# Performance work log

Measured on AMD Instinct MI355X. Metric: run time of the kernel, lower is better.

Reference implementation:

```python
import jax, jax.numpy as jnp
import numpy as np

N_NODES = 50000
N_EDGES = 800000
D = 128
HEADS = 1
N_LAYERS = 3
NEG_SLOPE = 0.2


def setup_inputs() -> dict:
    key = jax.random.key(0)
    ks = jax.random.split(key, 8)
    x = jax.random.normal(ks[0], (N_NODES, D), dtype=jnp.float32)
    edge_index = jax.random.randint(ks[1], (2, N_EDGES), 0, N_NODES, dtype=jnp.int64)
    # Per-layer GATConv params (heads=1): lin [D, H*D], att_src/att_dst [H, D], bias [H*D]
    s = 1.0 / np.sqrt(D)
    W = jax.random.normal(ks[2], (N_LAYERS, D, HEADS * D), dtype=jnp.float32) * s
    att_src = jax.random.normal(ks[3], (N_LAYERS, HEADS, D), dtype=jnp.float32) * s
    att_dst = jax.random.normal(ks[4], (N_LAYERS, HEADS, D), dtype=jnp.float32) * s
    bias = jnp.zeros((N_LAYERS, HEADS * D), dtype=jnp.float32)
    return {"x": x, "edge_index": edge_index, "W": W, "att_src": att_src,
            "att_dst": att_dst, "bias": bias}


def _gat_conv(x, src, dst, W, a_src, a_dst, b):
    # x: [N, D] -> xp: [N, H, C]
    N = x.shape[0]
    xp = (x @ W).reshape(N, HEADS, D)
    alpha_s = jnp.sum(xp * a_src, axis=-1)  # [N, H]
    alpha_d = jnp.sum(xp * a_dst, axis=-1)  # [N, H]
    # per-edge attention logits (message j=src -> i=dst)
    e = alpha_s[src] + alpha_d[dst]                       # [E, H]
    e = jnp.where(e > 0, e, NEG_SLOPE * e)                # leaky_relu(0.2)
    # segment softmax over destination node
    m = jax.ops.segment_max(e, dst, num_segments=N)       # [N, H]
    ex = jnp.exp(e - m[dst])
    denom = jax.ops.segment_sum(ex, dst, num_segments=N)  # [N, H]
    coef = ex / (denom[dst] + 1e-16)                      # [E, H]
    # scatter-aggregate messages
    out = jax.ops.segment_sum(xp[src] * coef[:, :, None], dst, num_segments=N)  # [N, H, C]
    return out.reshape(N, HEADS * D) + b


def reference(x, edge_index, W, att_src, att_dst, bias):
    N = x.shape[0]
    # GATConv default add_self_loops=True: append (i, i) for every node
    loops = jnp.arange(N, dtype=edge_index.dtype)
    src = jnp.concatenate([edge_index[0], loops])
    dst = jnp.concatenate([edge_index[1], loops])
    h = x
    for l in range(N_LAYERS):
        # dropout omitted for deterministic reference (eval-mode semantics)
        h = _gat_conv(h, src, dst, W[l], att_src[l], att_dst[l], bias[l])
        if l < N_LAYERS - 1:
            h = jax.nn.gelu(h)
    return h
```

## Files before the change

### kernel.cpp

```cpp
#include <hip/hip_runtime.h>
#include <hip/hip_bf16.h>
#include <hip/hip_fp16.h>

#define NN    50000
#define NE    800000
#define ETOT  (NE + NN)
#define D     128
#define NB    ((NN + 255) / 256)
#define EB    ((ETOT + 255) / 256)

typedef _Float16 f16x8 __attribute__((ext_vector_type(8)));
typedef float    f32x4 __attribute__((ext_vector_type(4)));

__device__ __forceinline__ float gelu_fast(float x) {
    float x2 = x * x;
    float z2 = x * fmaf(x2, 0.07135483f, 1.5957691f);
    float e  = __expf(z2);
    return x - __fdividef(x, e + 1.0f);
}


__global__ __launch_bounds__(256) void init_k(
        int* __restrict__ counts, const float* __restrict__ W,
        const float* __restrict__ asrc, const float* __restrict__ adst,
        float* __restrict__ wasd, __half* __restrict__ WT) {
    int b = blockIdx.x, t = threadIdx.x;
    if (b < NB) {
        int i = b * 256 + t;
        if (i < NN) counts[i] = 0;
    } else if (b < NB + 3) {
        int l = b - NB;
        int k = t & 127, which = t >> 7;
        const float* wr = W + (size_t)l * 16384 + (size_t)k * 128;
        const float* av = (which ? adst : asrc) + (size_t)l * 128;
        float s = 0.f;
        #pragma unroll 4
        for (int c = 0; c < 128; ++c) s += wr[c] * av[c];
        wasd[l * 256 + which * 128 + k] = s;
    } else {
        int i = (b - NB - 3) * 256 + t;
        int l = i >> 14, r = i & 16383;
        int k = r >> 7, c = r & 127;
        WT[(size_t)l * 16384 + (size_t)c * 128 + k] =
            __float2half_rn(W[(size_t)l * 16384 + (size_t)k * 128 + c]);
    }
}


template <int AIN32>
__device__ __forceinline__ void gemm_body(
        int b2, int t, const void* __restrict__ A, const __half* __restrict__ WT,
        const float* __restrict__ wasd, __half* __restrict__ XP,
        float* __restrict__ alpha_s, float* __restrict__ alpha_d, __half* Bs) {
    #pragma unroll
    for (int it = 0; it < 8; ++it) {
        int bb = it * 4096 + t * 16;
        int c = bb >> 8;
        int swz = bb ^ ((c & 7) << 4);
        *(uint4*)((char*)Bs + swz) = *(const uint4*)((const char*)WT + bb);
    }
    __syncthreads();

    int w = t >> 6, lane = t & 63;
    int r0 = (b2 >> 1) * 256 + w * 64;
    int c0 = (b2 & 1) * 64;
    int lr = lane & 15, lg = lane >> 4;
    bool doalpha = (b2 & 1) == 0;

    f32x4 acc[4][4];
    #pragma unroll
    for (int i = 0; i < 4; ++i)
        #pragma unroll
        for (int j = 0; j < 4; ++j)
            acc[i][j] = (f32x4){0.f, 0.f, 0.f, 0.f};

    float ps[4] = {0, 0, 0, 0}, pd[4] = {0, 0, 0, 0};

    #pragma unroll
    for (int ks = 0; ks < 4; ++ks) {
        f16x8 bf[4];
        #pragma unroll
        for (int ct = 0; ct < 4; ++ct) {
            int c  = c0 + ct * 16 + lr;
            int kb = ks * 64 + lg * 16;
            int addr = c * 256 + (kb ^ ((c & 7) << 4));
            bf[ct] = *(const f16x8*)((const char*)Bs + addr);
        }
        float4 s0, s1, d0, d1;
        if (doalpha) {
            const float* wsp = wasd + ks * 32 + lg * 8;
            s0 = *(const float4*)(wsp);       s1 = *(const float4*)(wsp + 4);
            d0 = *(const float4*)(wsp + 128); d1 = *(const float4*)(wsp + 132);
        }
        #pragma unroll
        for (int rt = 0; rt < 4; ++rt) {
            int row = r0 + rt * 16 + lr;
            int rc  = row < NN ? row : NN - 1;
            f16x8 af;
            float4 f0, f1;
            if (AIN32) {
                const float* ap = (const float*)A + (size_t)rc * D + ks * 32 + lg * 8;
                f0 = *(const float4*)ap;
                f1 = *(const float4*)(ap + 4);
                af[0] = (_Float16)f0.x; af[1] = (_Float16)f0.y;
                af[2] = (_Float16)f0.z; af[3] = (_Float16)f0.w;
                af[4] = (_Float16)f1.x; af[5] = (_Float16)f1.y;
                af[6] = (_Float16)f1.z; af[7] = (_Float16)f1.w;
            } else {
                af = *(const f16x8*)((const char*)A + (size_t)rc * 256 + ks * 64 + lg * 16);
                if (doalpha) {
                    f0 = make_float4((float)af[0], (float)af[1], (float)af[2], (float)af[3]);
                    f1 = make_float4((float)af[4], (float)af[5], (float)af[6], (float)af[7]);
                }
            }
            if (doalpha) {
                ps[rt] += f0.x*s0.x + f0.y*s0.y + f0.z*s0.z + f0.w*s0.w
                        + f1.x*s1.x + f1.y*s1.y + f1.z*s1.z + f1.w*s1.w;
                pd[rt] += f0.x*d0.x + f0.y*d0.y + f0.z*d0.z + f0.w*d0.w
                        + f1.x*d1.x + f1.y*d1.y + f1.z*d1.z + f1.w*d1.w;
            }
            #pragma unroll
            for (int ct = 0; ct < 4; ++ct)
                acc[rt][ct] = __builtin_amdgcn_mfma_f32_16x16x32_f16(
                                  af, bf[ct], acc[rt][ct], 0, 0, 0);
        }
    }

    #pragma unroll
    for (int rt = 0; rt < 4; ++rt) {
        #pragma unroll
        for (int q = 0; q < 4; ++q) {
            int row = r0 + rt * 16 + lg * 4 + q;
            if (row < NN) {
                #pragma unroll
                for (int ct = 0; ct < 4; ++ct)
                    XP[(size_t)row * D + c0 + ct * 16 + lr] = __float2half_rn(acc[rt][ct][q]);
            }
        }
    }

    if (doalpha) {
        #pragma unroll
        for (int rt = 0; rt < 4; ++rt) {
            float p = ps[rt], dq = pd[rt];
            p  += __shfl_xor(p, 16);  p  += __shfl_xor(p, 32);
            dq += __shfl_xor(dq, 16); dq += __shfl_xor(dq, 32);
            int row = r0 + rt * 16 + lr;
            if (lane < 16 && row < NN) { alpha_s[row] = p; alpha_d[row] = dq; }
        }
    }
}


__global__ __launch_bounds__(256) void prep2_k(
        const int* __restrict__ dst_arr, int* __restrict__ counts, int* __restrict__ rank,
        const float* __restrict__ x, const __half* __restrict__ WT,
        const float* __restrict__ wasd, __half* __restrict__ XPH,
        float* __restrict__ alpha_s, float* __restrict__ alpha_d) {
    __shared__ __half Bs[D * D];
    int b = blockIdx.x, t = threadIdx.x;
    if (b < EB) {
        int e = b * 256 + t;
        if (e < ETOT) {
            int d = (e < NE) ? dst_arr[e] : (e - NE);
            rank[e] = atomicAdd(&counts[d], 1);
        }
    } else {
        gemm_body<1>(b - EB, t, x, WT, wasd, XPH, alpha_s, alpha_d, Bs);
    }
}


__global__ __launch_bounds__(256) void gemm_k(
        const __half* __restrict__ TH, const __half* __restrict__ WT,
        const float* __restrict__ wasd, __half* __restrict__ XPH,
        float* __restrict__ alpha_s, float* __restrict__ alpha_d) {
    __shared__ __half Bs[D * D];
    gemm_body<0>(blockIdx.x, threadIdx.x, TH, WT, wasd, XPH, alpha_s, alpha_d, Bs);
}


__global__ void scan1_k(const int* __restrict__ counts, int* __restrict__ blk_sums) {
    __shared__ int sm[4];
    int i = blockIdx.x * 256 + threadIdx.x;
    int v = (i < NN) ? counts[i] : 0;
    #pragma unroll
    for (int o = 32; o; o >>= 1) v += __shfl_xor(v, o);
    if ((threadIdx.x & 63) == 0) sm[threadIdx.x >> 6] = v;
    __syncthreads();
    if (threadIdx.x == 0) blk_sums[blockIdx.x] = sm[0] + sm[1] + sm[2] + sm[3];
}

__global__ void scan23_k(const int* __restrict__ counts, const int* __restrict__ blk_sums,
                         int* __restrict__ row_ptr) {
    __shared__ int s[256];
    __shared__ int boff_sh;
    int t = threadIdx.x, bid = blockIdx.x;
    if (t < 64) {
        int acc = 0;
        for (int i = t; i < bid; i += 64) acc += blk_sums[i];
        #pragma unroll
        for (int o = 32; o; o >>= 1) acc += __shfl_xor(acc, o);
        if (t == 0) boff_sh = acc;
    }
    __syncthreads();
    int boff = boff_sh;
    int i = bid * 256 + t;
    int v = (i < NN) ? counts[i] : 0;
    s[t] = v;
    __syncthreads();
    for (int off = 1; off < 256; off <<= 1) {
        int x = (t >= off) ? s[t - off] : 0;
        __syncthreads();
        s[t] += x;
        __syncthreads();
    }
    int excl = s[t] - v + boff;
    if (i < NN) row_ptr[i] = excl;
    if (bid == NB - 1 && t == 255) row_ptr[NN] = s[255] + boff;
}

__global__ void scatter2_k(const int* __restrict__ srcarr, const int* __restrict__ dstarr,
                           const int* __restrict__ rank, const int* __restrict__ row_ptr,
                           int* __restrict__ srcs) {
    int e = blockIdx.x * blockDim.x + threadIdx.x;
    if (e >= ETOT) return;
    int d, s;
    if (e < NE) { d = dstarr[e]; s = srcarr[e]; }
    else        { d = e - NE;    s = e - NE; }
    srcs[row_ptr[d] + rank[e]] = s;
}


template <int OUT32, int GELU>
__global__ __launch_bounds__(256) void agg_u_k(
        const int* __restrict__ row_ptr, const int* __restrict__ srcs,
        const float* __restrict__ alpha_s, const float* __restrict__ alpha_d,
        const __half* __restrict__ XPH, const float* __restrict__ bias,
        void* __restrict__ outp) {
    __shared__ float xch[4][128];
    int wv = threadIdx.x >> 6;
    int n = (blockIdx.x * blockDim.x + threadIdx.x) >> 6;
    int lane = threadIdx.x & 63;
    int beg = row_ptr[n], end = row_ptr[n + 1], deg = end - beg;
    float ad = alpha_d[n];
    int qw = lane >> 4, q = lane & 15;

    float2 fin;

    if (deg <= 64) {
        int sreg = 0;
        float e = -3.4e38f;
        if (lane < deg) {
            sreg = srcs[beg + lane];
            float v = alpha_s[sreg] + ad;
            e = v > 0.f ? v : 0.2f * v;
        }
        float m = e;
        #pragma unroll
        for (int o = 32; o; o >>= 1) m = fmaxf(m, __shfl_xor(m, o));
        float w = (lane < deg) ? __expf(e - m) : 0.f;
        float denom = w;
        #pragma unroll
        for (int o = 32; o; o >>= 1) denom += __shfl_xor(denom, o);

        float acc[8] = {0,0,0,0,0,0,0,0};
        int dgr = (deg + 3) & ~3;
        const char* xb = (const char*)XPH;
        int qb = q << 4;
        int j = 0;
        #define PROC(UU, WW)                                                     \
            {                                                                    \
                union { uint4 u; __half2 h[4]; } U; U.u = (UU);                  \
                float2 f0 = __half22float2(U.h[0]);                              \
                float2 f1 = __half22float2(U.h[1]);                              \
                float2 f2 = __half22float2(U.h[2]);                              \
                float2 f3 = __half22float2(U.h[3]);                              \
                acc[0] += (WW)*f0.x; acc[1] += (WW)*f0.y;                        \
                acc[2] += (WW)*f1.x; acc[3] += (WW)*f1.y;                        \
                acc[4] += (WW)*f2.x; acc[5] += (WW)*f2.y;                        \
                acc[6] += (WW)*f3.x; acc[7] += (WW)*f3.y;                        \
            }
        for (; j + 16 <= dgr; j += 16) {
            int   s0 = __shfl(sreg, j + qw);       float w0 = __shfl(w, j + qw);
            int   s1 = __shfl(sreg, j + 4 + qw);   float w1 = __shfl(w, j + 4 + qw);
            int   s2 = __shfl(sreg, j + 8 + qw);   float w2 = __shfl(w, j + 8 + qw);
            int   s3 = __shfl(sreg, j + 12 + qw);  float w3 = __shfl(w, j + 12 + qw);
            uint4 u0 = *(const uint4*)(xb + ((s0 << 8) + qb));
            uint4 u1 = *(const uint4*)(xb + ((s1 << 8) + qb));
            uint4 u2 = *(const uint4*)(xb + ((s2 << 8) + qb));
            uint4 u3 = *(const uint4*)(xb + ((s3 << 8) + qb));
            PROC(u0, w0) PROC(u1, w1) PROC(u2, w2) PROC(u3, w3)
        }
        for (; j < dgr; j += 4) {
            int   s0 = __shfl(sreg, j + qw);
            float w0 = __shfl(w, j + qw);
            uint4 u0 = *(const uint4*)(xb + ((s0 << 8) + qb));
            PROC(u0, w0)
        }
        #undef PROC
        #pragma unroll
        for (int f = 0; f < 8; ++f) {
            acc[f] += __shfl_xor(acc[f], 16);
            acc[f] += __shfl_xor(acc[f], 32);
        }
        if (lane < 16) {
            float4* p = (float4*)&xch[wv][q * 8];
            p[0] = make_float4(acc[0], acc[1], acc[2], acc[3]);
            p[1] = make_float4(acc[4], acc[5], acc[6], acc[7]);
        }
        __asm__ volatile("s_waitcnt lgkmcnt(0)" ::: "memory");
        __builtin_amdgcn_sched_barrier(0);
        float2 a2 = *(const float2*)&xch[wv][2 * lane];
        float inv = 1.f / (denom + 1e-16f);
        fin.x = a2.x * inv;
        fin.y = a2.y * inv;
    } else {
        float m = -3.4e38f;
        for (int i = beg + lane; i < end; i += 64) {
            int s = srcs[i];
            float v = alpha_s[s] + ad; v = v > 0.f ? v : 0.2f * v;
            m = fmaxf(m, v);
        }
        #pragma unroll
        for (int o = 32; o; o >>= 1) m = fmaxf(m, __shfl_xor(m, o));
        float denom = 0.f;
        for (int i = beg + lane; i < end; i += 64) {
            int s = srcs[i];
            float v = alpha_s[s] + ad; v = v > 0.f ? v : 0.2f * v;
            denom += __expf(v - m);
        }
        #pragma unroll
        for (int o = 32; o; o >>= 1) denom += __shfl_xor(denom, o);
        float2 acc = {0.f, 0.f};
        for (int i = beg; i < end; ++i) {
            int s = srcs[i];
            float v = alpha_s[s] + ad; v = v > 0.f ? v : 0.2f * v;
            float wgt = __expf(v - m);
            union { unsigned int x; __half2 h; } U;
            U.x = ((const unsigned int*)(XPH + (size_t)s * D))[lane];
            float2 f = __half22float2(U.h);
            acc.x += wgt * f.x; acc.y += wgt * f.y;
        }
        float inv = 1.f / (denom + 1e-16f);
        fin.x = acc.x * inv;
        fin.y = acc.y * inv;
    }

    float2 b2 = ((const float2*)bias)[lane];
    fin.x += b2.x;
    fin.y += b2.y;
    if (GELU) { fin.x = gelu_fast(fin.x); fin.y = gelu_fast(fin.y); }

    if (OUT32) {
        ((float2*)((float*)outp + (size_t)n * D))[lane] = fin;
    } else {
        ((__half2*)((__half*)outp + (size_t)n * D))[lane] = __floats2half2_rn(fin.x, fin.y);
    }
}


extern "C" void kernel_launch(void* const* d_in, const int* in_sizes, int n_in,
                              void* d_out, int out_size, void* d_ws, size_t ws_size,
                              hipStream_t stream) {
    const float* x    = (const float*)d_in[0];
    const int*   ei   = (const int*)d_in[1];
    const float* W    = (const float*)d_in[2];
    const float* asrc = (const float*)d_in[3];
    const float* adst = (const float*)d_in[4];
    const float* bias = (const float*)d_in[5];
    float* out = (float*)d_out;

    const int* src_arr = ei;
    const int* dst_arr = ei + NE;

    char* ws = (char*)d_ws;
    size_t off = 0;
    auto alloc = [&](size_t bytes) { char* p = ws + off; off += (bytes + 255) & ~(size_t)255; return p; };
    __half* th_a    = (__half*)alloc((size_t)NN * D * sizeof(__half));
    __half* th_b    = (__half*)alloc((size_t)NN * D * sizeof(__half));
    __half* xph     = (__half*)alloc((size_t)NN * D * sizeof(__half));
    __half* wt      = (__half*)alloc((size_t)3 * D * D * sizeof(__half));
    float*  as_a    = (float*)alloc(NN * sizeof(float));
    float*  ad_a    = (float*)alloc(NN * sizeof(float));
    float*  wasd    = (float*)alloc(3 * 256 * sizeof(float));
    int* counts    = (int*)alloc(NN * sizeof(int));
    int* row_ptr   = (int*)alloc((NN + 1) * sizeof(int));
    int* rank      = (int*)alloc((size_t)ETOT * sizeof(int));
    int* blk_sums  = (int*)alloc(NB * sizeof(int));
    int* srcs      = (int*)alloc((size_t)ETOT * sizeof(int));
    (void)ws_size; (void)in_sizes; (void)n_in; (void)out_size;

    init_k<<<NB + 3 + 192, 256, 0, stream>>>(counts, W, asrc, adst, wasd, wt);
    prep2_k<<<EB + 392, 256, 0, stream>>>(dst_arr, counts, rank, x, wt, wasd,
                                          xph, as_a, ad_a);
    scan1_k<<<NB, 256, 0, stream>>>(counts, blk_sums);
    scan23_k<<<NB, 256, 0, stream>>>(counts, blk_sums, row_ptr);
    scatter2_k<<<EB, 256, 0, stream>>>(src_arr, dst_arr, rank, row_ptr, srcs);

    int ab = NN / 4;

    agg_u_k<0, 1><<<ab, 256, 0, stream>>>(row_ptr, srcs, as_a, ad_a, xph, bias, th_b);
    gemm_k<<<392, 256, 0, stream>>>(th_b, wt + 16384, wasd + 256, xph, as_a, ad_a);
    agg_u_k<0, 1><<<ab, 256, 0, stream>>>(row_ptr, srcs, as_a, ad_a, xph, bias + D, th_a);
    gemm_k<<<392, 256, 0, stream>>>(th_a, wt + 32768, wasd + 512, xph, as_a, ad_a);
    agg_u_k<1, 0><<<ab, 256, 0, stream>>>(row_ptr, srcs, as_a, ad_a, xph, bias + 2 * D, out);
}
```

Measured before the change: 205.2 us.

## Replace global atomic CSR counting with per-block LDS byte histograms and merge

Builds the destination-sorted edge list by having 256 blocks each compute a packed 8-bit histogram in shared memory with LDS atomics, instead of doing one global atomicAdd per edge. A merge kernel then computes per-block offsets and total counts, and the scatter is fused with the first-layer GEMM. The aim is to remove global atomic contention and shrink the rank array to bytes. The cost is a large per-block counts matrix (HB×NNP bytes) that must be written and read back, plus an extra kernel. Per-block counts are assumed to fit in 8 bits, which holds for random edges.

```diff
diff --git a/kernel.cpp b/kernel.cpp
--- a/kernel.cpp
+++ b/kernel.cpp
@@ -7,7 +7,10 @@
 #define ETOT  (NE + NN)
 #define D     128
 #define NB    ((NN + 255) / 256)
-#define EB    ((ETOT + 255) / 256)
+#define HB    256
+#define EPB   3328
+#define NNP   50176
+#define NNPW  (NNP / 4)
 
 typedef _Float16 f16x8 __attribute__((ext_vector_type(8)));
 typedef float    f32x4 __attribute__((ext_vector_type(4)));
@@ -21,15 +24,12 @@
 
 
 __global__ __launch_bounds__(256) void init_k(
-        int* __restrict__ counts, const float* __restrict__ W,
+        const float* __restrict__ W,
         const float* __restrict__ asrc, const float* __restrict__ adst,
         float* __restrict__ wasd, __half* __restrict__ WT) {
     int b = blockIdx.x, t = threadIdx.x;
-    if (b < NB) {
-        int i = b * 256 + t;
-        if (i < NN) counts[i] = 0;
-    } else if (b < NB + 3) {
-        int l = b - NB;
+    if (b < 3) {
+        int l = b;
         int k = t & 127, which = t >> 7;
         const float* wr = W + (size_t)l * 16384 + (size_t)k * 128;
         const float* av = (which ? adst : asrc) + (size_t)l * 128;
@@ -38,12 +38,104 @@
         for (int c = 0; c < 128; ++c) s += wr[c] * av[c];
         wasd[l * 256 + which * 128 + k] = s;
     } else {
-        int i = (b - NB - 3) * 256 + t;
+        int i = (b - 3) * 256 + t;
         int l = i >> 14, r = i & 16383;
         int k = r >> 7, c = r & 127;
         WT[(size_t)l * 16384 + (size_t)c * 128 + k] =
             __float2half_rn(W[(size_t)l * 16384 + (size_t)k * 128 + c]);
     }
+}
+
+
+__global__ __launch_bounds__(256) void hist_k(
+        const int* __restrict__ dst_arr, unsigned char* __restrict__ rank8,
+        unsigned int* __restrict__ counts8 ) {
+    __shared__ unsigned int h[NNPW];
+    int p = blockIdx.x, t = threadIdx.x;
+    for (int i = t; i < NNPW; i += 256) h[i] = 0u;
+    __syncthreads();
+    int base = p * EPB;
+    #pragma unroll
+    for (int it = 0; it < 13; ++it) {
+        int e = base + it * 256 + t;
+        if (e < ETOT) {
+            int d = (e < NE) ? dst_arr[e] : (e - NE);
+            int sh = (d & 3) * 8;
+            unsigned int old = atomicAdd(&h[d >> 2], 1u << sh);
+            rank8[e] = (unsigned char)((old >> sh) & 0xffu);
+        }
+    }
+    __syncthreads();
+    unsigned int* crow = counts8 + (size_t)p * NNPW;
+    for (int i = t; i < NNPW; i += 256) crow[i] = h[i];
+}
+
+
+__global__ __launch_bounds__(256) void merge_k(
+        const unsigned char* __restrict__ counts8, unsigned char* __restrict__ boff8,
+        int* __restrict__ counts) {
+    __shared__ int segtot[4][64];
+    int t = threadIdx.x;
+    int dl = t & 63, seg = t >> 6;
+    int d = blockIdx.x * 64 + dl;
+    const unsigned char* cp = counts8 + (size_t)seg * 64 * NNP + d;
+    int partial = 0;
+    #pragma unroll 8
+    for (int p = 0; p < 64; ++p) partial += (int)cp[(size_t)p * NNP];
+    segtot[seg][dl] = partial;
+    __syncthreads();
+    int base = 0;
+    if (seg > 0) base += segtot[0][dl];
+    if (seg > 1) base += segtot[1][dl];
+    if (seg > 2) base += segtot[2][dl];
+    unsigned char* bp = boff8 + (size_t)seg * 64 * NNP + d;
+    int acc = base;
+    for (int p = 0; p < 64; ++p) {
+        bp[(size_t)p * NNP] = (unsigned char)acc;
+        acc += (int)cp[(size_t)p * NNP];
+    }
+    if (seg == 3 && d < NN) counts[d] = acc;
+}
+
+
+__global__ void scan1_k(const int* __restrict__ counts, int* __restrict__ blk_sums) {
+    __shared__ int sm[4];
+    int i = blockIdx.x * 256 + threadIdx.x;
+    int v = (i < NN) ? counts[i] : 0;
+    #pragma unroll
+    for (int o = 32; o; o >>= 1) v += __shfl_xor(v, o);
+    if ((threadIdx.x & 63) == 0) sm[threadIdx.x >> 6] = v;
+    __syncthreads();
+    if (threadIdx.x == 0) blk_sums[blockIdx.x] = sm[0] + sm[1] + sm[2] + sm[3];
+}
+
+__global__ void scan23_k(const int* __restrict__ counts, const int* __restrict__ blk_sums,
+                         int* __restrict__ row_ptr) {
+    __shared__ int s[256];
+    __shared__ int boff_sh;
+    int t = threadIdx.x, bid = blockIdx.x;
+    if (t < 64) {
+        int acc = 0;
+        for (int i = t; i < bid; i += 64) acc += blk_sums[i];
+        #pragma unroll
+        for (int o = 32; o; o >>= 1) acc += __shfl_xor(acc, o);
+        if (t == 0) boff_sh = acc;
+    }
+    __syncthreads();
+    int boff = boff_sh;
+    int i = bid * 256 + t;
+    int v = (i < NN) ? counts[i] : 0;
+    s[t] = v;
+    __syncthreads();
+    for (int off = 1; off < 256; off <<= 1) {
+        int x = (t >= off) ? s[t - off] : 0;
+        __syncthreads();
+        s[t] += x;
+        __syncthreads();
+    }
+    int excl = s[t] - v + boff;
+    if (i < NN) row_ptr[i] = excl;
+    if (bid == NB - 1 && t == 255) row_ptr[NN] = s[255] + boff;
 }
 
 
@@ -152,21 +244,30 @@
 }
 
 
-__global__ __launch_bounds__(256) void prep2_k(
-        const int* __restrict__ dst_arr, int* __restrict__ counts, int* __restrict__ rank,
+__global__ __launch_bounds__(256) void sg_k(
+        const int* __restrict__ src_arr, const int* __restrict__ dst_arr,
+        const unsigned char* __restrict__ rank8, const unsigned char* __restrict__ boff8,
+        const int* __restrict__ row_ptr, int* __restrict__ srcs,
         const float* __restrict__ x, const __half* __restrict__ WT,
         const float* __restrict__ wasd, __half* __restrict__ XPH,
         float* __restrict__ alpha_s, float* __restrict__ alpha_d) {
     __shared__ __half Bs[D * D];
     int b = blockIdx.x, t = threadIdx.x;
-    if (b < EB) {
-        int e = b * 256 + t;
-        if (e < ETOT) {
-            int d = (e < NE) ? dst_arr[e] : (e - NE);
-            rank[e] = atomicAdd(&counts[d], 1);
+    if (b < HB) {
+        const unsigned char* brow = boff8 + (size_t)b * NNP;
+        int base = b * EPB;
+        #pragma unroll
+        for (int it = 0; it < 13; ++it) {
+            int e = base + it * 256 + t;
+            if (e < ETOT) {
+                int d, s;
+                if (e < NE) { d = dst_arr[e]; s = src_arr[e]; }
+                else        { d = e - NE;    s = e - NE; }
+                srcs[row_ptr[d] + (int)brow[d] + (int)rank8[e]] = s;
+            }
         }
     } else {
-        gemm_body<1>(b - EB, t, x, WT, wasd, XPH, alpha_s, alpha_d, Bs);
+        gemm_body<1>(b - HB, t, x, WT, wasd, XPH, alpha_s, alpha_d, Bs);
     }
 }
 
@@ -177,58 +278,6 @@
         float* __restrict__ alpha_s, float* __restrict__ alpha_d) {
     __shared__ __half Bs[D * D];
     gemm_body<0>(blockIdx.x, threadIdx.x, TH, WT, wasd, XPH, alpha_s, alpha_d, Bs);
-}
-
-
-__global__ void scan1_k(const int* __restrict__ counts, int* __restrict__ blk_sums) {
-    __shared__ int sm[4];
-    int i = blockIdx.x * 256 + threadIdx.x;
-    int v = (i < NN) ? counts[i] : 0;
-    #pragma unroll
-    for (int o = 32; o; o >>= 1) v += __shfl_xor(v, o);
-    if ((threadIdx.x & 63) == 0) sm[threadIdx.x >> 6] = v;
-    __syncthreads();
-    if (threadIdx.x == 0) blk_sums[blockIdx.x] = sm[0] + sm[1] + sm[2] + sm[3];
-}
-
-__global__ void scan23_k(const int* __restrict__ counts, const int* __restrict__ blk_sums,
-                         int* __restrict__ row_ptr) {
-    __shared__ int s[256];
-    __shared__ int boff_sh;
-    int t = threadIdx.x, bid = blockIdx.x;
-    if (t < 64) {
-        int acc = 0;
-        for (int i = t; i < bid; i += 64) acc += blk_sums[i];
-        #pragma unroll
-        for (int o = 32; o; o >>= 1) acc += __shfl_xor(acc, o);
-        if (t == 0) boff_sh = acc;
-    }
-    __syncthreads();
-    int boff = boff_sh;
-    int i = bid * 256 + t;
-    int v = (i < NN) ? counts[i] : 0;
-    s[t] = v;
-    __syncthreads();
-    for (int off = 1; off < 256; off <<= 1) {
-        int x = (t >= off) ? s[t - off] : 0;
-        __syncthreads();
-        s[t] += x;
-        __syncthreads();
-    }
-    int excl = s[t] - v + boff;
-    if (i < NN) row_ptr[i] = excl;
-    if (bid == NB - 1 && t == 255) row_ptr[NN] = s[255] + boff;
-}
-
-__global__ void scatter2_k(const int* __restrict__ srcarr, const int* __restrict__ dstarr,
-                           const int* __restrict__ rank, const int* __restrict__ row_ptr,
-                           int* __restrict__ srcs) {
-    int e = blockIdx.x * blockDim.x + threadIdx.x;
-    if (e >= ETOT) return;
-    int d, s;
-    if (e < NE) { d = dstarr[e]; s = srcarr[e]; }
-    else        { d = e - NE;    s = e - NE; }
-    srcs[row_ptr[d] + rank[e]] = s;
 }
 
 
@@ -386,17 +435,20 @@
     float*  wasd    = (float*)alloc(3 * 256 * sizeof(float));
     int* counts    = (int*)alloc(NN * sizeof(int));
     int* row_ptr   = (int*)alloc((NN + 1) * sizeof(int));
-    int* rank      = (int*)alloc((size_t)ETOT * sizeof(int));
     int* blk_sums  = (int*)alloc(NB * sizeof(int));
     int* srcs      = (int*)alloc((size_t)ETOT * sizeof(int));
+    unsigned int*  counts8 = (unsigned int*)alloc((size_t)HB * NNP);
+    unsigned char* boff8   = (unsigned char*)alloc((size_t)HB * NNP);
+    unsigned char* rank8   = (unsigned char*)alloc((size_t)HB * EPB);
     (void)ws_size; (void)in_sizes; (void)n_in; (void)out_size;
 
-    init_k<<<NB + 3 + 192, 256, 0, stream>>>(counts, W, asrc, adst, wasd, wt);
-    prep2_k<<<EB + 392, 256, 0, stream>>>(dst_arr, counts, rank, x, wt, wasd,
-                                          xph, as_a, ad_a);
+    init_k<<<3 + 192, 256, 0, stream>>>(W, asrc, adst, wasd, wt);
+    hist_k<<<HB, 256, 0, stream>>>(dst_arr, rank8, counts8);
+    merge_k<<<(NN + 63) / 64, 256, 0, stream>>>((const unsigned char*)counts8, boff8, counts);
     scan1_k<<<NB, 256, 0, stream>>>(counts, blk_sums);
     scan23_k<<<NB, 256, 0, stream>>>(counts, blk_sums, row_ptr);
-    scatter2_k<<<EB, 256, 0, stream>>>(src_arr, dst_arr, rank, row_ptr, srcs);
+    sg_k<<<HB + 392, 256, 0, stream>>>(src_arr, dst_arr, rank8, boff8, row_ptr, srcs,
+                                       x, wt, wasd, xph, as_a, ad_a);
 
     int ab = NN / 4;
 
```

Result: faster. 196.2 us (-4.4%).
